# Performance work log

Measured on AMD Instinct MI355X. Metric: run time of the kernel, lower is better.

The kernel has to match this reference:

```python
import jax, jax.numpy as jnp
import numpy as np

N_NODES = 131072
B_GRAPHS = 16
L_MAX = 8192  # nodes per graph (equal partition -> static dense shape)
CHANNELS = 512
HEAD_CH = 128  # head_channels, heads fixed to 1


def _to_dense_batch(x, batch, num_graphs, max_nodes):
    # Mirrors torch_geometric.utils.to_dense_batch for a sorted batch vector.
    n = x.shape[0]
    counts = jnp.zeros((num_graphs,), jnp.int32).at[batch].add(1)
    offsets = jnp.concatenate([jnp.zeros((1,), jnp.int32), jnp.cumsum(counts)[:-1]])
    pos = jnp.arange(n, dtype=jnp.int32) - offsets[batch]
    dense = jnp.zeros((num_graphs, max_nodes, x.shape[1]), x.dtype).at[batch, pos].set(x)
    mask = jnp.zeros((num_graphs, max_nodes), bool).at[batch, pos].set(True)
    return dense, mask


def setup_inputs() -> dict:
    key = jax.random.key(0)
    kx, kq, kk, kv = jax.random.split(key, 4)
    x = jax.random.normal(kx, (N_NODES, CHANNELS), jnp.float32)
    scale = 1.0 / np.sqrt(CHANNELS)
    Wq = jax.random.normal(kq, (HEAD_CH, CHANNELS), jnp.float32) * scale
    Wk = jax.random.normal(kk, (HEAD_CH, CHANNELS), jnp.float32) * scale
    Wv = jax.random.normal(kv, (HEAD_CH, CHANNELS), jnp.float32) * scale
    # sorted batch vector: equal-size graphs so L_MAX is static
    batch = (jnp.arange(N_NODES, dtype=jnp.int32) // L_MAX).astype(jnp.int32)
    return {"x": x, "Wq": Wq, "Wk": Wk, "Wv": Wv, "batch": batch,
            "num_graphs": B_GRAPHS, "max_nodes": L_MAX}


def reference(x, Wq, Wk, Wv, batch, num_graphs, max_nodes):
    B, L, H, M = num_graphs, max_nodes, 1, Wq.shape[0]
    xd, mask = _to_dense_batch(x, batch, B, L)  # [B, L, C]; padded rows are zero
    qs = (xd @ Wq.T).reshape(B, L, H, M)
    ks = (xd @ Wk.T).reshape(B, L, H, M)
    vs = (xd @ Wv.T).reshape(B, L, H, M)
    # GLOBAL (scalar) Frobenius norm, as in torch.norm(t, p=2)
    qs = qs / jnp.linalg.norm(qs)
    ks = ks / jnp.linalg.norm(ks)
    n_const = qs.shape[0]  # source uses qs.shape[0] (= batch size) here
    # linear attention: K^T V first, then Q (K^T V)
    kvs = jnp.einsum('blhm,blhd->bhmd', ks, vs)
    attention_num = jnp.einsum('bnhm,bhmd->bnhd', qs, kvs) + n_const * vs
    ks_sum = ks.sum(axis=1)  # [B, H, M]
    attention_normalizer = jnp.einsum('bnhm,bhm->bnh', qs, ks_sum)[..., None] + n_const
    attn_output = attention_num / attention_normalizer  # [B, L, H, M]
    return attn_output
```

## Files before the change

### kernel.cpp

```cpp
#include <hip/hip_runtime.h>
#include <hip/hip_bf16.h>

typedef __bf16 bf16;
typedef __bf16 bf16x4 __attribute__((ext_vector_type(4)));
typedef __bf16 bf16x8 __attribute__((ext_vector_type(8)));
typedef float f32x4 __attribute__((ext_vector_type(4)));

#define N_NODES 131072
#define CH      512
#define HD      128
#define LMAX    8192
#define NG      16

typedef __attribute__((address_space(3))) unsigned int lds_u32;
typedef __attribute__((address_space(1))) const unsigned int g_u32;

__device__ __forceinline__ void gload16(const void* gp, void* lp) {
    __builtin_amdgcn_global_load_lds((g_u32*)gp, (lds_u32*)lp, 16, 0, 0);
}

__global__ __launch_bounds__(256, 1) void k0_prep(
    const float* __restrict__ Wq, const float* __restrict__ Wk,
    const float* __restrict__ Wv, bf16* __restrict__ wsW)
{
    int t = blockIdx.x * 256 + threadIdx.x;
    int c = t / 1536;
    int r = t % 1536;
    int j = r >> 2, g = r & 3;
    const float* Wrow = (j < 128) ? (Wq + (size_t)j * CH)
                       : (j < 256) ? (Wk + (size_t)(j - 128) * CH)
                                   : (Wv + (size_t)(j - 256) * CH);
    int col0 = c * 32 + ((g ^ ((j >> 1) & 3)) << 3);
    float4 f0 = *(const float4*)(Wrow + col0);
    float4 f1 = *(const float4*)(Wrow + col0 + 4);
    bf16x8 o;
    o[0] = (bf16)f0.x; o[1] = (bf16)f0.y; o[2] = (bf16)f0.z; o[3] = (bf16)f0.w;
    o[4] = (bf16)f1.x; o[5] = (bf16)f1.y; o[6] = (bf16)f1.z; o[7] = (bf16)f1.w;
    *(bf16x8*)(wsW + (size_t)t * 8) = o;
}

__global__ __launch_bounds__(256, 2) void k1_proj(
    const float* __restrict__ x, const bf16* __restrict__ wsW,
    bf16* __restrict__ qo, bf16* __restrict__ ko, bf16* __restrict__ vo,
    float* __restrict__ sumsq)
{
    __shared__ bf16 As[2][64][40];
    __shared__ bf16 Bs[12288];
    __shared__ float rq[4], rk[4];

    const int tid = threadIdx.x;
    const int lane = tid & 63;
    const int w = tid >> 6;
    const int lr = lane & 15, lh = lane >> 4;
    const int n0 = blockIdx.x * 64;
    const int ar = tid >> 3, ac = tid & 7;

    f32x4 acc[4][6];
    #pragma unroll
    for (int mi = 0; mi < 4; mi++)
        #pragma unroll
        for (int ni = 0; ni < 6; ni++)
            acc[mi][ni] = (f32x4){0.f, 0.f, 0.f, 0.f};

    float4 areg0, areg1;

    {
        const char* wb = (const char*)wsW + w * 1024 + lane * 16;
        char* db = (char*)Bs + w * 1024;
        #pragma unroll
        for (int i = 0; i < 6; i++) gload16(wb + i * 4096, db + i * 4096);
        areg0 = *(const float4*)(x + (size_t)(n0 + ar) * CH + ac * 4);
        areg1 = *(const float4*)(x + (size_t)(n0 + ar + 32) * CH + ac * 4);
        bf16x4 t0, t1;
        t0[0] = (bf16)areg0.x; t0[1] = (bf16)areg0.y; t0[2] = (bf16)areg0.z; t0[3] = (bf16)areg0.w;
        t1[0] = (bf16)areg1.x; t1[1] = (bf16)areg1.y; t1[2] = (bf16)areg1.z; t1[3] = (bf16)areg1.w;
        *(bf16x4*)&As[0][ar][ac * 4] = t0;
        *(bf16x4*)&As[0][ar + 32][ac * 4] = t1;
        __syncthreads();
    }

    for (int c = 0; c < 16; c++) {
        const int cur = c & 1, nxt = cur ^ 1;
        if (c < 15) {
            areg0 = *(const float4*)(x + (size_t)(n0 + ar) * CH + (c + 1) * 32 + ac * 4);
            areg1 = *(const float4*)(x + (size_t)(n0 + ar + 32) * CH + (c + 1) * 32 + ac * 4);
        }
        bf16x8 af[4];
        #pragma unroll
        for (int mi = 0; mi < 4; mi++)
            af[mi] = *(const bf16x8*)&As[cur][mi * 16 + lr][lh * 8];
        #pragma unroll
        for (int mi = 0; mi < 4; mi++) {
            #pragma unroll
            for (int ni = 0; ni < 6; ni++) {
                int j = w * 96 + ni * 16 + lr;
                int g = lh ^ ((j >> 1) & 3);
                bf16x8 bf_ = *(const bf16x8*)&Bs[j * 32 + (g << 3)];
                acc[mi][ni] = __builtin_amdgcn_mfma_f32_16x16x32_bf16(
                    af[mi], bf_, acc[mi][ni], 0, 0, 0);
            }
        }
        if (c < 15) {
            bf16x4 t0, t1;
            t0[0] = (bf16)areg0.x; t0[1] = (bf16)areg0.y; t0[2] = (bf16)areg0.z; t0[3] = (bf16)areg0.w;
            t1[0] = (bf16)areg1.x; t1[1] = (bf16)areg1.y; t1[2] = (bf16)areg1.z; t1[3] = (bf16)areg1.w;
            *(bf16x4*)&As[nxt][ar][ac * 4] = t0;
            *(bf16x4*)&As[nxt][ar + 32][ac * 4] = t1;
        }
        __syncthreads();
        if (c < 15) {
            const char* wb = (const char*)wsW + (size_t)(c + 1) * 24576 + w * 1024 + lane * 16;
            char* db = (char*)Bs + w * 1024;
            #pragma unroll
            for (int i = 0; i < 6; i++) gload16(wb + i * 4096, db + i * 4096);
            __syncthreads();
        }
    }

    float sq = 0.f, sk = 0.f;
    #pragma unroll
    for (int mi = 0; mi < 4; mi++) {
        #pragma unroll
        for (int ni = 0; ni < 6; ni++) {
            int col = w * 96 + ni * 16 + lr;
            int arr = col >> 7, cc = col & 127;
            bf16* dst = (arr == 0) ? qo : (arr == 1) ? ko : vo;
            #pragma unroll
            for (int r = 0; r < 4; r++) {
                int row = n0 + mi * 16 + lh * 4 + r;
                float val = acc[mi][ni][r];
                dst[(size_t)row * HD + cc] = (bf16)val;
                if (arr == 0) sq += val * val;
                else if (arr == 1) sk += val * val;
            }
        }
    }
    #pragma unroll
    for (int off = 32; off > 0; off >>= 1) {
        sq += __shfl_down(sq, off);
        sk += __shfl_down(sk, off);
    }
    if (lane == 0) { rq[w] = sq; rk[w] = sk; }
    __syncthreads();
    if (tid == 0) {
        float a = 0.f, b = 0.f;
        #pragma unroll
        for (int i = 0; i < 4; i++) { a += rq[i]; b += rk[i]; }
        atomicAdd(&sumsq[0], a);
        atomicAdd(&sumsq[1], b);
    }
}

__global__ __launch_bounds__(512, 1) void k2_kv(
    const bf16* __restrict__ ko, const bf16* __restrict__ vo,
    float* __restrict__ part_kv, float* __restrict__ part_ks)
{
    __shared__ __align__(16) char smem[16640];
    bf16 (*kt)[130] = (bf16(*)[130])smem;
    bf16 (*vt)[130] = (bf16(*)[130])(smem + 8320);
    float* scr = (float*)smem;

    const int tid = threadIdx.x, lane = tid & 63, w = tid >> 6;
    const int wr = w >> 2, wc = w & 3;
    const int lr = lane & 15, lh = lane >> 4;
    const int b = blockIdx.x >> 4, cch = blockIdx.x & 15;
    const size_t l0 = (size_t)b * LMAX + (size_t)cch * 512;
    const int sr = tid >> 4, sc = tid & 15;

    f32x4 acc[4][2];
    #pragma unroll
    for (int mi = 0; mi < 4; mi++)
        #pragma unroll
        for (int ni = 0; ni < 2; ni++)
            acc[mi][ni] = (f32x4){0.f, 0.f, 0.f, 0.f};
    float ks8[8] = {};

    uint4 kk4 = *(const uint4*)&ko[(l0 + sr) * HD + sc * 8];
    uint4 vv4 = *(const uint4*)&vo[(l0 + sr) * HD + sc * 8];

    for (int lt = 0; lt < 512; lt += 32) {
        __syncthreads();
        #pragma unroll
        for (int j2 = 0; j2 < 4; j2++) {
            *(unsigned int*)&kt[sr][sc * 8 + j2 * 2] = ((const unsigned int*)&kk4)[j2];
            *(unsigned int*)&vt[sr][sc * 8 + j2 * 2] = ((const unsigned int*)&vv4)[j2];
        }
        #pragma unroll
        for (int j = 0; j < 8; j++) ks8[j] += (float)((const bf16*)&kk4)[j];
        __syncthreads();
        if (lt + 32 < 512) {
            kk4 = *(const uint4*)&ko[(l0 + lt + 32 + sr) * HD + sc * 8];
            vv4 = *(const uint4*)&vo[(l0 + lt + 32 + sr) * HD + sc * 8];
        }
        bf16x8 a[4], bb[2];
        #pragma unroll
        for (int mi = 0; mi < 4; mi++) {
            int m = wr * 64 + mi * 16 + lr;
            #pragma unroll
            for (int j = 0; j < 8; j++) a[mi][j] = kt[lh * 8 + j][m];
        }
        #pragma unroll
        for (int ni = 0; ni < 2; ni++) {
            int d = wc * 32 + ni * 16 + lr;
            #pragma unroll
            for (int j = 0; j < 8; j++) bb[ni][j] = vt[lh * 8 + j][d];
        }
        #pragma unroll
        for (int mi = 0; mi < 4; mi++)
            #pragma unroll
            for (int ni = 0; ni < 2; ni++)
                acc[mi][ni] = __builtin_amdgcn_mfma_f32_16x16x32_bf16(
                    a[mi], bb[ni], acc[mi][ni], 0, 0, 0);
    }

    __syncthreads();
    #pragma unroll
    for (int j = 0; j < 8; j++) scr[tid * 8 + j] = ks8[j];
    __syncthreads();
    if (tid < 128) {
        float s = 0.f;
        #pragma unroll
        for (int g = 0; g < 32; g++)
            s += scr[((g << 4) | (tid >> 3)) * 8 + (tid & 7)];
        part_ks[blockIdx.x * HD + tid] = s;
    }

    float* dst = part_kv + (size_t)blockIdx.x * 16384;
    #pragma unroll
    for (int mi = 0; mi < 4; mi++)
        #pragma unroll
        for (int ni = 0; ni < 2; ni++)
            #pragma unroll
            for (int r = 0; r < 4; r++) {
                int m = wr * 64 + mi * 16 + lh * 4 + r;
                int d = wc * 32 + ni * 16 + lr;
                dst[m * HD + d] = acc[mi][ni][r];
            }
}

__global__ __launch_bounds__(256, 1) void k2b_reduce(
    const float* __restrict__ part_kv, const float* __restrict__ part_ks,
    const float* __restrict__ sumsq,
    bf16* __restrict__ kvsT, float* __restrict__ ks_sum_s)
{
    const int b = blockIdx.x >> 3, ms = blockIdx.x & 7, tid = threadIdx.x;
    const float s_qk = rsqrtf(sumsq[0]) * rsqrtf(sumsq[1]);

    #pragma unroll
    for (int i = 0; i < 8; i++) {
        int idx = i * 256 + tid;
        int m = ms * 16 + (idx >> 7), d = idx & 127;
        float s = 0.f;
        #pragma unroll
        for (int c = 0; c < 16; c++)
            s += part_kv[((size_t)(b * 16 + c) << 14) + (m << 7) + d];
        kvsT[((size_t)b << 14) + (d << 7) + m] = (bf16)(s * s_qk);
    }
    if (ms == 0 && tid < 128) {
        float s = 0.f;
        #pragma unroll
        for (int c = 0; c < 16; c++)
            s += part_ks[(b * 16 + c) * HD + tid];
        ks_sum_s[b * HD + tid] = s * s_qk;
    }
}

__global__ __launch_bounds__(256, 2) void k3_out(
    const bf16* __restrict__ qo, const bf16* __restrict__ vo,
    const bf16* __restrict__ kvsT, const float* __restrict__ ks_sum_s,
    float* __restrict__ out)
{
    __shared__ bf16 qs[128][136];
    __shared__ bf16 vsh[128][136];
    __shared__ float kss[128];
    __shared__ float denom[128];
    const int tid = threadIdx.x, lane = tid & 63, w = tid >> 6;
    const int lr = lane & 15, lh = lane >> 4;
    const int n0 = blockIdx.x * 128;
    const int b = n0 >> 13;

    #pragma unroll
    for (int i = 0; i < 8; i++) {
        int idx = tid + i * 256;
        int r = idx >> 4, c8 = idx & 15;
        *(bf16x8*)&qs[r][c8 * 8]  = *(const bf16x8*)&qo[(size_t)(n0 + r) * HD + c8 * 8];
        *(bf16x8*)&vsh[r][c8 * 8] = *(const bf16x8*)&vo[(size_t)(n0 + r) * HD + c8 * 8];
    }
    if (tid < 128) kss[tid] = ks_sum_s[b * HD + tid];
    __syncthreads();

    if (tid < 128) {
        float s = 0.f;
        #pragma unroll 8
        for (int m = 0; m < HD; m++) s += (float)qs[tid][m] * kss[m];
        denom[tid] = s + 16.0f;
    }

    f32x4 acc[2][8];
    #pragma unroll
    for (int mi = 0; mi < 2; mi++)
        #pragma unroll
        for (int ni = 0; ni < 8; ni++)
            acc[mi][ni] = (f32x4){0.f, 0.f, 0.f, 0.f};

    #pragma unroll
    for (int k0 = 0; k0 < HD; k0 += 32) {
        bf16x8 a[2], bb[8];
        #pragma unroll
        for (int mi = 0; mi < 2; mi++)
            a[mi] = *(const bf16x8*)&qs[w * 32 + mi * 16 + lr][k0 + lh * 8];
        #pragma unroll
        for (int ni = 0; ni < 8; ni++)
            bb[ni] = *(const bf16x8*)&kvsT[(size_t)b * 16384 + (size_t)(ni * 16 + lr) * HD + k0 + lh * 8];
        #pragma unroll
        for (int mi = 0; mi < 2; mi++)
            #pragma unroll
            for (int ni = 0; ni < 8; ni++)
                acc[mi][ni] = __builtin_amdgcn_mfma_f32_16x16x32_bf16(
                    a[mi], bb[ni], acc[mi][ni], 0, 0, 0);
    }
    __syncthreads();

    #pragma unroll
    for (int mi = 0; mi < 2; mi++) {
        #pragma unroll
        for (int ni = 0; ni < 8; ni++) {
            int col = ni * 16 + lr;
            #pragma unroll
            for (int r = 0; r < 4; r++) {
                int row = w * 32 + mi * 16 + lh * 4 + r;
                float vv = (float)vsh[row][col];
                out[(size_t)(n0 + row) * HD + col] =
                    (acc[mi][ni][r] + 16.0f * vv) / denom[row];
            }
        }
    }
}

extern "C" void kernel_launch(void* const* d_in, const int* in_sizes, int n_in,
                              void* d_out, int out_size, void* d_ws, size_t ws_size,
                              hipStream_t stream)
{
    const float* x  = (const float*)d_in[0];
    const float* Wq = (const float*)d_in[1];
    const float* Wk = (const float*)d_in[2];
    const float* Wv = (const float*)d_in[3];

    char* ws = (char*)d_ws;
    const size_t Q_OFF   = 0;
    const size_t K_OFF   = 33554432;
    const size_t V_OFF   = 67108864;
    const size_t PKV_OFF = 100663296;
    const size_t PKS_OFF = 117440512;
    const size_t KVS_OFF = 117571584;
    const size_t KSS_OFF = 118095872;
    const size_t SSQ_OFF = 118104064;
    const size_t NEED    = 118104072;
    if (ws_size < NEED) return;

    bf16*  qo      = (bf16*)(ws + Q_OFF);
    bf16*  ko      = (bf16*)(ws + K_OFF);
    bf16*  vo      = (bf16*)(ws + V_OFF);
    float* part_kv = (float*)(ws + PKV_OFF);
    float* part_ks = (float*)(ws + PKS_OFF);
    bf16*  kvsT    = (bf16*)(ws + KVS_OFF);
    float* ks_sum  = (float*)(ws + KSS_OFF);
    float* sumsq   = (float*)(ws + SSQ_OFF);
    bf16*  wsW     = (bf16*)(ws + PKV_OFF);

    hipMemsetAsync(sumsq, 0, 8, stream);
    k0_prep<<<dim3(96), dim3(256), 0, stream>>>(Wq, Wk, Wv, wsW);
    k1_proj<<<dim3(N_NODES / 64), dim3(256), 0, stream>>>(x, wsW, qo, ko, vo, sumsq);
    k2_kv<<<dim3(256), dim3(512), 0, stream>>>(ko, vo, part_kv, part_ks);
    k2b_reduce<<<dim3(128), dim3(256), 0, stream>>>(part_kv, part_ks, sumsq, kvsT, ks_sum);
    k3_out<<<dim3(N_NODES / 128), dim3(256), 0, stream>>>(qo, vo, kvsT, ks_sum, (float*)d_out);
}
```

Before: 204.5 us.

## Stream fp32 x tiles into LDS via direct loads and widen weight K-chunk

The projection kernel now loads the fp32 x tile directly into LDS with global_load_lds, double-buffered and XOR-swizzled. The bf16 conversion moves to the point where the MFMA fragments are read, replacing the register staging and LDS store path. Weight chunks grow to 64 K-columns with a new 8-way swizzle, so B tiles reload every other iteration, and the MFMA loop is reordered to reuse each B fragment across the M tiles. LDS use roughly doubles and launch bounds drop to 1 block per SM, which costs occupancy.

Result: slower. 209.9 us (+2.6%).

```diff
diff --git a/kernel.cpp b/kernel.cpp
--- a/kernel.cpp
+++ b/kernel.cpp
@@ -24,28 +24,29 @@
     const float* __restrict__ Wv, bf16* __restrict__ wsW)
 {
     int t = blockIdx.x * 256 + threadIdx.x;
-    int c = t / 1536;
-    int r = t % 1536;
-    int j = r >> 2, g = r & 3;
+    int c = t / 3072;
+    int r = t % 3072;
+    int j = r >> 3, g = r & 7;
     const float* Wrow = (j < 128) ? (Wq + (size_t)j * CH)
                        : (j < 256) ? (Wk + (size_t)(j - 128) * CH)
                                    : (Wv + (size_t)(j - 256) * CH);
-    int col0 = c * 32 + ((g ^ ((j >> 1) & 3)) << 3);
-    float4 f0 = *(const float4*)(Wrow + col0);
-    float4 f1 = *(const float4*)(Wrow + col0 + 4);
+    int col0 = (g ^ (j & 7)) << 3;
+    const float* src = Wrow + c * 64 + col0;
+    float4 f0 = *(const float4*)src;
+    float4 f1 = *(const float4*)(src + 4);
     bf16x8 o;
     o[0] = (bf16)f0.x; o[1] = (bf16)f0.y; o[2] = (bf16)f0.z; o[3] = (bf16)f0.w;
     o[4] = (bf16)f1.x; o[5] = (bf16)f1.y; o[6] = (bf16)f1.z; o[7] = (bf16)f1.w;
     *(bf16x8*)(wsW + (size_t)t * 8) = o;
 }
 
-__global__ __launch_bounds__(256, 2) void k1_proj(
+__global__ __launch_bounds__(256, 1) void k1_proj(
     const float* __restrict__ x, const bf16* __restrict__ wsW,
     bf16* __restrict__ qo, bf16* __restrict__ ko, bf16* __restrict__ vo,
     float* __restrict__ sumsq)
 {
-    __shared__ bf16 As[2][64][40];
-    __shared__ bf16 Bs[12288];
+    __shared__ float A32[2][2048];
+    __shared__ bf16 Bs[24576];
     __shared__ float rq[4], rk[4];
 
     const int tid = threadIdx.x;
@@ -53,7 +54,10 @@
     const int w = tid >> 6;
     const int lr = lane & 15, lh = lane >> 4;
     const int n0 = blockIdx.x * 64;
-    const int ar = tid >> 3, ac = tid & 7;
+
+    const int as_row = lane >> 3;
+    const int as_col = (((lane & 7) ^ as_row) << 2);
+    const size_t abase = (size_t)(n0 + as_row) * CH + as_col;
 
     f32x4 acc[4][6];
     #pragma unroll
@@ -61,58 +65,60 @@
         #pragma unroll
         for (int ni = 0; ni < 6; ni++)
             acc[mi][ni] = (f32x4){0.f, 0.f, 0.f, 0.f};
-
-    float4 areg0, areg1;
 
     {
         const char* wb = (const char*)wsW + w * 1024 + lane * 16;
         char* db = (char*)Bs + w * 1024;
         #pragma unroll
-        for (int i = 0; i < 6; i++) gload16(wb + i * 4096, db + i * 4096);
-        areg0 = *(const float4*)(x + (size_t)(n0 + ar) * CH + ac * 4);
-        areg1 = *(const float4*)(x + (size_t)(n0 + ar + 32) * CH + ac * 4);
-        bf16x4 t0, t1;
-        t0[0] = (bf16)areg0.x; t0[1] = (bf16)areg0.y; t0[2] = (bf16)areg0.z; t0[3] = (bf16)areg0.w;
-        t1[0] = (bf16)areg1.x; t1[1] = (bf16)areg1.y; t1[2] = (bf16)areg1.z; t1[3] = (bf16)areg1.w;
-        *(bf16x4*)&As[0][ar][ac * 4] = t0;
-        *(bf16x4*)&As[0][ar + 32][ac * 4] = t1;
+        for (int i = 0; i < 12; i++) gload16(wb + i * 4096, db + i * 4096);
+        #pragma unroll
+        for (int i = 0; i < 2; i++) {
+            int jc = w * 2 + i;
+            gload16((const char*)(x + abase + (size_t)jc * 8 * CH),
+                    (char*)&A32[0][jc * 256]);
+        }
         __syncthreads();
     }
 
-    for (int c = 0; c < 16; c++) {
-        const int cur = c & 1, nxt = cur ^ 1;
-        if (c < 15) {
-            areg0 = *(const float4*)(x + (size_t)(n0 + ar) * CH + (c + 1) * 32 + ac * 4);
-            areg1 = *(const float4*)(x + (size_t)(n0 + ar + 32) * CH + (c + 1) * 32 + ac * 4);
+    for (int a = 0; a < 16; a++) {
+        const int cur = a & 1, nxt = cur ^ 1;
+        const int kk = (a & 1) * 32;
+        if (a < 15) {
+            #pragma unroll
+            for (int i = 0; i < 2; i++) {
+                int jc = w * 2 + i;
+                gload16((const char*)(x + abase + (size_t)jc * 8 * CH + (a + 1) * 32),
+                        (char*)&A32[nxt][jc * 256]);
+            }
         }
         bf16x8 af[4];
         #pragma unroll
-        for (int mi = 0; mi < 4; mi++)
-            af[mi] = *(const bf16x8*)&As[cur][mi * 16 + lr][lh * 8];
-        #pragma unroll
         for (int mi = 0; mi < 4; mi++) {
-            #pragma unroll
-            for (int ni = 0; ni < 6; ni++) {
-                int j = w * 96 + ni * 16 + lr;
-                int g = lh ^ ((j >> 1) & 3);
-                bf16x8 bf_ = *(const bf16x8*)&Bs[j * 32 + (g << 3)];
+            int r = mi * 16 + lr;
+            int base = r * 32;
+            f32x4 lo = *(const f32x4*)&A32[cur][base + ((( lh * 2     ) ^ (lr & 7)) << 2)];
+            f32x4 hi = *(const f32x4*)&A32[cur][base + (((lh * 2 + 1) ^ (lr & 7)) << 2)];
+            bf16x8 t;
+            t[0] = (bf16)lo[0]; t[1] = (bf16)lo[1]; t[2] = (bf16)lo[2]; t[3] = (bf16)lo[3];
+            t[4] = (bf16)hi[0]; t[5] = (bf16)hi[1]; t[6] = (bf16)hi[2]; t[7] = (bf16)hi[3];
+            af[mi] = t;
+        }
+        #pragma unroll
+        for (int ni = 0; ni < 6; ni++) {
+            int j = w * 96 + ni * 16 + lr;
+            bf16x8 bf_ = *(const bf16x8*)&Bs[j * 64 + ((kk + lh * 8) ^ ((j & 7) << 3))];
+            #pragma unroll
+            for (int mi = 0; mi < 4; mi++)
                 acc[mi][ni] = __builtin_amdgcn_mfma_f32_16x16x32_bf16(
                     af[mi], bf_, acc[mi][ni], 0, 0, 0);
-            }
-        }
-        if (c < 15) {
-            bf16x4 t0, t1;
-            t0[0] = (bf16)areg0.x; t0[1] = (bf16)areg0.y; t0[2] = (bf16)areg0.z; t0[3] = (bf16)areg0.w;
-            t1[0] = (bf16)areg1.x; t1[1] = (bf16)areg1.y; t1[2] = (bf16)areg1.z; t1[3] = (bf16)areg1.w;
-            *(bf16x4*)&As[nxt][ar][ac * 4] = t0;
-            *(bf16x4*)&As[nxt][ar + 32][ac * 4] = t1;
         }
         __syncthreads();
-        if (c < 15) {
-            const char* wb = (const char*)wsW + (size_t)(c + 1) * 24576 + w * 1024 + lane * 16;
+        if ((a & 1) && a < 15) {
+            const char* wb = (const char*)wsW + (size_t)((a >> 1) + 1) * 49152
+                           + w * 1024 + lane * 16;
             char* db = (char*)Bs + w * 1024;
             #pragma unroll
-            for (int i = 0; i < 6; i++) gload16(wb + i * 4096, db + i * 4096);
+            for (int i = 0; i < 12; i++) gload16(wb + i * 4096, db + i * 4096);
             __syncthreads();
         }
     }
```
